# Performance work log

Measured on AMD Instinct MI355X. Metric: run time of the kernel, lower is better.

The kernel has to match this reference:

```python
import jax, jax.numpy as jnp
import numpy as np

B, N, E, D = 2, 8192, 1024, 128   # batch, seq, embed_dim, expand_ratio (= head dim)
H = E // D                        # 8 heads (f_proj output dim)
CHUNK = 64
LN_EPS = 1e-5


def _gla_chunked(q, k, v, log_f):
    """Chunked simple GLA: S_t = exp(log_f_t) * S_{t-1} + k_t v_t^T ; o_t = q_t @ S_t.
    q,k,v: [b,h,n,d], log_f: [b,h,n] (log of per-head scalar decay in (0,1))."""
    b, h, n, d = q.shape
    nc = n // CHUNK
    qc = q.reshape(b, h, nc, CHUNK, d)
    kc = k.reshape(b, h, nc, CHUNK, d)
    vc = v.reshape(b, h, nc, CHUNK, d)
    gf = log_f.reshape(b, h, nc, CHUNK)
    g = jnp.cumsum(gf, axis=-1)          # inclusive within-chunk cum log decay [b,h,nc,C]
    gl = g[..., -1]                      # total chunk log decay [b,h,nc]

    # intra-chunk: A[i,j] = (q_i . k_j) * exp(g_i - g_j), j <= i  (g decreasing -> stable)
    mask = jnp.tril(jnp.ones((CHUNK, CHUNK), bool))
    A = jnp.einsum('bhcid,bhcjd->bhcij', qc, kc)
    A = jnp.where(mask, A * jnp.exp(g[..., :, None] - g[..., None, :]), 0.0)
    o_intra = jnp.einsum('bhcij,bhcjd->bhcid', A, vc)

    # inter-chunk: scan over chunks carrying state S [b,h,d,d]
    def step(S, inp):
        q_c, k_c, v_c, g_c, gl_c = inp   # [b,h,C,d],[b,h,C,d],[b,h,C,d],[b,h,C],[b,h]
        o = jnp.einsum('bhid,bhde->bhie', q_c * jnp.exp(g_c)[..., None], S)
        kd = k_c * jnp.exp(gl_c[..., None] - g_c)[..., None]
        S = jnp.exp(gl_c)[..., None, None] * S + jnp.einsum('bhid,bhie->bhde', kd, v_c)
        return S, o

    xs = (jnp.moveaxis(qc, 2, 0), jnp.moveaxis(kc, 2, 0), jnp.moveaxis(vc, 2, 0),
          jnp.moveaxis(g, 2, 0), jnp.moveaxis(gl, 2, 0))
    S0 = jnp.zeros((b, h, d, d), q.dtype)
    _, o_inter = jax.lax.scan(step, S0, xs)      # [nc,b,h,C,d]
    o_inter = jnp.moveaxis(o_inter, 0, 2)        # [b,h,nc,C,d]
    return (o_intra + o_inter).reshape(b, h, n, d)


def setup_inputs() -> dict:
    key = jax.random.key(0)
    ks = jax.random.split(key, 13)
    s = E ** -0.5
    x = jax.random.normal(ks[0], (B, N, E), jnp.float32)
    # per-head lower bound in (0,1), stored in log space as consumed by the module
    log_lower_bound = jnp.log(jax.random.uniform(ks[1], (H,), jnp.float32, 0.05, 0.95))
    Wq = jax.random.normal(ks[2], (E, E), jnp.float32) * s
    Wk = jax.random.normal(ks[3], (E, E), jnp.float32) * s
    Wv = jax.random.normal(ks[4], (E, E), jnp.float32) * s
    Wf = jax.random.normal(ks[5], (E, H), jnp.float32) * s
    Wb1 = jax.random.normal(ks[6], (E, D), jnp.float32) * s
    Wb2 = jax.random.normal(ks[7], (D, E), jnp.float32) * (D ** -0.5)
    Wg1 = jax.random.normal(ks[8], (E, D), jnp.float32) * s
    Wg2 = jax.random.normal(ks[9], (D, E), jnp.float32) * (D ** -0.5)
    Wo = jax.random.normal(ks[10], (E, E), jnp.float32) * s
    ln_scale = jnp.ones((E,), jnp.float32)
    ln_bias = jnp.zeros((E,), jnp.float32)
    return dict(x=x, log_lower_bound=log_lower_bound, Wq=Wq, Wk=Wk, Wv=Wv, Wf=Wf,
                Wb1=Wb1, Wb2=Wb2, Wg1=Wg1, Wg2=Wg2, Wo=Wo,
                ln_scale=ln_scale, ln_bias=ln_bias)


def reference(x, log_lower_bound, Wq, Wk, Wv, Wf, Wb1, Wb2, Wg1, Wg2, Wo, ln_scale, ln_bias):
    silu = jax.nn.silu
    q = silu(x @ Wq)
    k = silu(x @ Wk)
    v = x @ Wv
    f_pre = x @ Wf                               # [B,N,H] per-head decay logits

    # dense-memory Householder-style reflection of q
    beta = silu((x @ Wb1) @ Wb2)
    nb = jnp.sqrt(jnp.sum(beta * beta, axis=-1, keepdims=True))
    beta = beta / jnp.maximum(nb, 1e-6) / (E ** 0.5)
    q = q - 2.0 * jnp.sum(q * beta, axis=-1, keepdims=True) * beta

    def split(t):
        return t.reshape(B, N, H, D).transpose(0, 2, 1, 3)   # [B,H,N,D]
    qh, kh, vh = split(q), split(k), split(v)

    lb = jnp.exp(log_lower_bound)                            # [H]
    f = lb + (1.0 - lb) * jax.nn.sigmoid(f_pre)              # [B,N,H]
    log_f = jnp.log(f).transpose(0, 2, 1)                    # [B,H,N]

    o = _gla_chunked(qh, kh, vh, log_f)                      # [B,H,N,D]
    o = o.transpose(0, 2, 1, 3).reshape(B, N, E)

    gate = jax.nn.sigmoid((x @ Wg1) @ Wg2)
    o = o * gate

    mu = jnp.mean(o, axis=-1, keepdims=True)
    var = jnp.var(o, axis=-1, keepdims=True)
    o = (o - mu) / jnp.sqrt(var + LN_EPS) * ln_scale + ln_bias
    return o @ Wo
```

## Files before the change

kernel.cpp:

```cpp
#include <hip/hip_runtime.h>
#include <hip/hip_bf16.h>
#include <cstdint>


using u16 = unsigned short;
using u32 = unsigned int;
using u64 = unsigned long long;

typedef __attribute__((ext_vector_type(8))) short s16x8;
typedef __attribute__((ext_vector_type(4))) float f32x4;

__device__ __forceinline__ float b2f(u16 b){ u32 u = ((u32)b)<<16; return __builtin_bit_cast(float,u); }
__device__ __forceinline__ u16 f2b(float f){
  u32 u = __builtin_bit_cast(u32,f);
  return (u16)((u + 0x7FFFu + ((u>>16)&1u)) >> 16);
}
__device__ __forceinline__ float sigm(float x){ return 1.f/(1.f + __expf(-x)); }
__device__ __forceinline__ float silu(float x){ return x * sigm(x); }

__device__ __forceinline__ void gload16(const void* g, void* l){
  __builtin_amdgcn_global_load_lds((const __attribute__((address_space(1))) void*)g,
                                   (__attribute__((address_space(3))) void*)l, 16, 0, 0);
}
#define MFMA(a,b,c) __builtin_amdgcn_mfma_f32_16x16x32_bf16((a),(b),(c),0,0,0)

__device__ __forceinline__ void bar(){
  asm volatile("" ::: "memory");
  __builtin_amdgcn_s_barrier();
  asm volatile("" ::: "memory");
}
__device__ __forceinline__ void wv4(){
  asm volatile("s_waitcnt vmcnt(4)" ::: "memory");
  __builtin_amdgcn_sched_barrier(0);
}
__device__ __forceinline__ void wv0(){
  asm volatile("s_waitcnt vmcnt(0)" ::: "memory");
  __builtin_amdgcn_sched_barrier(0);
}
__device__ __forceinline__ void wv8(){
  asm volatile("s_waitcnt vmcnt(8)" ::: "memory");
  __builtin_amdgcn_sched_barrier(0);
}

__device__ __forceinline__ void swz_block(int& bx, int& by){
  const int gx = gridDim.x;
  const int nwg = gx * gridDim.y;
  int lin = by*gx + bx;
  const int cpx = nwg >> 3;
  lin = (lin & 7)*cpx + (lin >> 3);
  bx = lin % gx; by = lin / gx;
}

__global__ __launch_bounds__(256) void fill_diag(float* __restrict__ p, int n, float val){
  int i = blockIdx.x*256 + threadIdx.x;
  if (i < n) p[i] = val;
}

__global__ __launch_bounds__(256) void cast_bf(const float4* __restrict__ src,
                                               ushort4* __restrict__ dst, int n4){
  int i = blockIdx.x*256 + threadIdx.x;
  int st = gridDim.x*256;
  for (; i < n4; i += st){
    float4 v = src[i];
    ushort4 o; o.x=f2b(v.x); o.y=f2b(v.y); o.z=f2b(v.z); o.w=f2b(v.w);
    dst[i] = o;
  }
}

__global__ __launch_bounds__(256) void wprep_all(const float* __restrict__ Wq,
                                                 const float* __restrict__ Wk,
                                                 const float* __restrict__ Wv,
                                                 const float* __restrict__ Wf,
                                                 const float* __restrict__ Wb1,
                                                 const float* __restrict__ Wb2,
                                                 const float* __restrict__ Wg1,
                                                 const float* __restrict__ Wg2,
                                                 const float* __restrict__ Wo,
                                                 u16* __restrict__ WCAT,
                                                 u16* __restrict__ WB2T,
                                                 u16* __restrict__ WG2T,
                                                 u16* __restrict__ WOT){
  const int z = blockIdx.z;
  const float* src; u16* dst; int K, Nsrc, kb, nb;
  switch(z){
    case 0: src=Wq;  dst=WCAT;            K=1024; Nsrc=1024; kb=16; nb=16; break;
    case 1: src=Wk;  dst=WCAT+1024*1024;  K=1024; Nsrc=1024; kb=16; nb=16; break;
    case 2: src=Wv;  dst=WCAT+2048*1024;  K=1024; Nsrc=1024; kb=16; nb=16; break;
    case 3: src=Wb1; dst=WCAT+3072*1024;  K=1024; Nsrc=128;  kb=16; nb=2;  break;
    case 4: src=Wg1; dst=WCAT+3200*1024;  K=1024; Nsrc=128;  kb=16; nb=2;  break;
    case 5: src=Wf;  dst=WCAT+3328*1024;  K=1024; Nsrc=8;    kb=16; nb=2;  break;
    case 6: src=Wb2; dst=WB2T;            K=128;  Nsrc=1024; kb=2;  nb=16; break;
    case 7: src=Wg2; dst=WG2T;            K=128;  Nsrc=1024; kb=2;  nb=16; break;
    default:src=Wo;  dst=WOT;             K=1024; Nsrc=1024; kb=16; nb=16; break;
  }
  if (blockIdx.x >= (u32)kb || blockIdx.y >= (u32)nb) return;
  __shared__ float t[64][65];
  const int k0 = blockIdx.x*64, n0 = blockIdx.y*64;
  const int tid = threadIdx.x;
  #pragma unroll
  for (int e=0;e<16;e++){
    int idx = e*256 + tid;
    int r = idx>>6, c = idx&63;
    float v = 0.f;
    if (n0 + c < Nsrc) v = src[(u64)(k0+r)*Nsrc + n0 + c];
    t[r][c] = v;
  }
  __syncthreads();
  #pragma unroll
  for (int e=0;e<16;e++){
    int idx = e*256 + tid;
    int nn = idx>>6, kk = idx&63;
    dst[(u64)(n0+nn)*K + k0 + kk] = f2b(t[kk][nn]);
  }
}

__global__ __launch_bounds__(256,4) void gemm_bt(const u16* __restrict__ A, int lda,
                                                 const u16* __restrict__ Bt,
                                                 void* __restrict__ C, int ldc,
                                                 int K, int mode){
  __shared__ __align__(16) u16 As[128*64];
  __shared__ __align__(16) u16 Bs[128*64];
  const int tid = threadIdx.x, lane = tid&63, wid = tid>>6;
  int bx = blockIdx.x, by = blockIdx.y;
  swz_block(bx, by);
  const int bn0 = bx*128, bm0 = by*128;
  const int wr = wid>>1, wc = wid&1;
  const int g = lane>>4, ln = lane&15;

  f32x4 acc[4][4];
  #pragma unroll
  for (int i=0;i<4;i++)
    #pragma unroll
    for (int j=0;j<4;j++) acc[i][j] = f32x4{0.f,0.f,0.f,0.f};

  const int nk = K >> 6;
  for (int kt = 0; kt < nk; ++kt){
    const int k0 = kt<<6;
    #pragma unroll
    for (int j=0;j<4;j++){
      const int p = (wid*4+j)*64 + lane;
      const int row = p>>3, sl = p&7;
      const int sc = ((sl ^ (row&7))<<3);
      gload16(A  + (u64)(bm0+row)*lda + k0 + sc, (char*)As + (wid*4+j)*1024);
      gload16(Bt + (u64)(bn0+row)*K   + k0 + sc, (char*)Bs + (wid*4+j)*1024);
    }
    __syncthreads();
    #pragma unroll
    for (int ks=0;ks<2;ks++){
      s16x8 af[4], bf[4];
      #pragma unroll
      for (int mt=0;mt<4;mt++){
        const int row = wr*64 + mt*16 + ln;
        af[mt] = *(const s16x8*)(As + row*64 + (((ks*4+g) ^ (row&7))<<3));
      }
      #pragma unroll
      for (int nt=0;nt<4;nt++){
        const int row = wc*64 + nt*16 + ln;
        bf[nt] = *(const s16x8*)(Bs + row*64 + (((ks*4+g) ^ (row&7))<<3));
      }
      #pragma unroll
      for (int mt=0;mt<4;mt++)
        #pragma unroll
        for (int nt=0;nt<4;nt++)
          acc[mt][nt] = MFMA(af[mt], bf[nt], acc[mt][nt]);
    }
    __syncthreads();
  }
  if (mode == 0){
    float* Cf = (float*)C;
    #pragma unroll
    for (int mt=0;mt<4;mt++)
      #pragma unroll
      for (int nt=0;nt<4;nt++){
        const int col = bn0 + wc*64 + nt*16 + ln;
        #pragma unroll
        for (int r=0;r<4;r++)
          Cf[(u64)(bm0 + wr*64 + mt*16 + g*4 + r)*ldc + col] = acc[mt][nt][r];
      }
  } else {
    u16* Cb = (u16*)C;
    #pragma unroll
    for (int mt=0;mt<4;mt++)
      #pragma unroll
      for (int nt=0;nt<4;nt++){
        const int col = bn0 + wc*64 + nt*16 + ln;
        #pragma unroll
        for (int r=0;r<4;r++)
          Cb[(u64)(bm0 + wr*64 + mt*16 + g*4 + r)*ldc + col] = f2b(acc[mt][nt][r]);
      }
  }
}

#define STAGE_H(kt_, b_, gb_, ld_, grow0_, loff_)                              \
  do{ const int kk0_ = (kt_)<<6;                                               \
    _Pragma("unroll")                                                          \
    for (int j_=0;j_<2;j_++){                                                  \
      const int p_ = j_*512 + tid;                                             \
      const int row_ = p_>>3, sl_ = p_&7;                                      \
      const int sc_ = ((sl_ ^ (row_&7))<<3);                                   \
      gload16((gb_) + (u64)((grow0_)+row_)*(ld_) + kk0_ + sc_,                 \
              (char*)lds + (b_)*65536 + (loff_) + j_*8192 + wid*1024);         \
    } }while(0)

#define PHASE(mh_, nh_, W_, SG_)                                               \
  do{                                                                          \
    if (W_) wv4();                                                             \
    bar();                                                                     \
    const u16* Ab_ = lds + cbuf*32768 + (mh_)*8192;                            \
    const u16* Bb_ = lds + cbuf*32768 + 16384 + (nh_)*8192;                    \
    s16x8 af_[2][4], bf_[2][2];                                                \
    _Pragma("unroll")                                                          \
    for (int ks=0;ks<2;ks++){                                                  \
      _Pragma("unroll")                                                        \
      for (int m=0;m<4;m++){                                                   \
        const int r_ = wr*64 + m*16 + ln;                                      \
        af_[ks][m] = *(const s16x8*)(Ab_ + r_*64 + (((ks*4+g) ^ (r_&7))<<3));  \
      }                                                                        \
      _Pragma("unroll")                                                        \
      for (int n=0;n<2;n++){                                                   \
        const int r_ = wc*32 + n*16 + ln;                                      \
        bf_[ks][n] = *(const s16x8*)(Bb_ + r_*64 + (((ks*4+g) ^ (r_&7))<<3));  \
      }                                                                        \
    }                                                                          \
    SG_;                                                                       \
    __builtin_amdgcn_s_setprio(1);                                             \
    _Pragma("unroll")                                                          \
    for (int ks=0;ks<2;ks++)                                                   \
      _Pragma("unroll")                                                        \
      for (int m=0;m<4;m++)                                                    \
        _Pragma("unroll")                                                      \
        for (int n=0;n<2;n++)                                                  \
          acc[(mh_)*4+m][(nh_)*2+n] =                                          \
            MFMA(af_[ks][m], bf_[ks][n], acc[(mh_)*4+m][(nh_)*2+n]);           \
    __builtin_amdgcn_s_setprio(0);                                             \
  }while(0)

#define GEMM8P_CORE()                                                          \
  f32x4 acc[8][4];                                                             \
  _Pragma("unroll")                                                            \
  for (int i=0;i<8;i++)                                                        \
    _Pragma("unroll")                                                          \
    for (int j=0;j<4;j++) acc[i][j] = f32x4{0.f,0.f,0.f,0.f};                  \
  const int nk = K >> 6;                                                       \
  STAGE_H(0,0,Bt,K,  bn0,     32768);                                          \
  STAGE_H(0,0,A, lda,bm0,     0);                                              \
  STAGE_H(0,0,Bt,K,  bn0+128, 49152);                                          \
  STAGE_H(0,0,A, lda,bm0+128, 16384);                                          \
  for (int kt=0; kt<nk-1; ++kt){                                               \
    const int cbuf = kt&1, nb = cbuf^1;                                        \
    PHASE(0,0,1, STAGE_H(kt+1,nb,Bt,K,  bn0,     32768));                      \
    PHASE(0,1,1, STAGE_H(kt+1,nb,A, lda,bm0,     0));                          \
    PHASE(1,1,1, STAGE_H(kt+1,nb,Bt,K,  bn0+128, 49152));                      \
    PHASE(1,0,0, STAGE_H(kt+1,nb,A, lda,bm0+128, 16384));                      \
  }                                                                            \
  { const int cbuf = (nk-1)&1;                                                 \
    wv0();                                                                     \
    PHASE(0,0,0,);                                                             \
    PHASE(0,1,0,);                                                             \
    PHASE(1,1,0,);                                                             \
    PHASE(1,0,0,); }

__global__ __launch_bounds__(512,2) void gemm256(const u16* __restrict__ A, int lda,
                                                 const u16* __restrict__ Bt,
                                                 void* __restrict__ C, int ldc,
                                                 int K, int mode){
  __shared__ __align__(16) u16 lds[2*32768];
  const int tid = threadIdx.x, lane = tid&63, wid = tid>>6;
  int bx = blockIdx.x, by = blockIdx.y;
  swz_block(bx, by);
  const int bn0 = bx*256, bm0 = by*256;
  const int wr = (wid>>2), wc = wid&3;
  const int g = lane>>4, ln = lane&15;
  GEMM8P_CORE();
  if (mode == 0){
    float* Cf = (float*)C;
    #pragma unroll
    for (int mh=0;mh<2;mh++)
      #pragma unroll
      for (int m=0;m<4;m++)
        #pragma unroll
        for (int nh=0;nh<2;nh++)
          #pragma unroll
          for (int n=0;n<2;n++){
            const int col = bn0 + nh*128 + wc*32 + n*16 + ln;
            #pragma unroll
            for (int r=0;r<4;r++)
              Cf[(u64)(bm0 + mh*128 + wr*64 + m*16 + g*4 + r)*ldc + col] =
                acc[mh*4+m][nh*2+n][r];
          }
  } else {
    u16* Cb = (u16*)C;
    #pragma unroll
    for (int mh=0;mh<2;mh++)
      #pragma unroll
      for (int m=0;m<4;m++)
        #pragma unroll
        for (int nh=0;nh<2;nh++)
          #pragma unroll
          for (int n=0;n<2;n++){
            const int col = bn0 + nh*128 + wc*32 + n*16 + ln;
            #pragma unroll
            for (int r=0;r<4;r++)
              Cb[(u64)(bm0 + mh*128 + wr*64 + m*16 + g*4 + r)*ldc + col] =
                f2b(acc[mh*4+m][nh*2+n][r]);
          }
  }
}

__global__ __launch_bounds__(512,2) void gemm_proj(const u16* __restrict__ A,
                                                   const u16* __restrict__ Bt,
                                                   u16* __restrict__ Qb,
                                                   u16* __restrict__ Kp,
                                                   u16* __restrict__ KT,
                                                   u16* __restrict__ VT,
                                                   u16* __restrict__ FP,
                                                   const float* __restrict__ Gp,
                                                   const float* __restrict__ GLp){
  __shared__ __align__(16) u16 lds[2*32768];
  const int tid = threadIdx.x, lane = tid&63, wid = tid>>6;
  int bx = blockIdx.x, by = blockIdx.y;
  swz_block(bx, by);
  const int bn0 = bx*256, bm0 = by*256;
  const int lda = 1024, K = 1024;
  const int wr = (wid>>2), wc = wid&3;
  const int g = lane>>4, ln = lane&15;
  GEMM8P_CORE();

  #pragma unroll
  for (int nh=0;nh<2;nh++){
    const int hb2 = (bn0>>7) + nh;
    if (hb2 < 8){
      #pragma unroll
      for (int mh=0;mh<2;mh++)
        #pragma unroll
        for (int m=0;m<4;m++)
          #pragma unroll
          for (int n=0;n<2;n++){
            const int col = bn0 + nh*128 + wc*32 + n*16 + ln;
            #pragma unroll
            for (int r=0;r<4;r++)
              Qb[(u64)(bm0 + mh*128 + wr*64 + m*16 + g*4 + r)*1024 + col] =
                f2b(acc[mh*4+m][nh*2+n][r]);
          }
    } else if (hb2 < 16){
      const int h = hb2 - 8;
      const int bh = (bm0>>13)*8 + h;
      #pragma unroll
      for (int mh=0;mh<2;mh++)
        #pragma unroll
        for (int m=0;m<4;m++){
          const int trowb = (bm0&8191) + mh*128 + wr*64 + m*16 + g*4;
          const float gl = GLp[bh*128 + (trowb>>6)];
          float es[4];
          #pragma unroll
          for (int r=0;r<4;r++) es[r] = __expf(gl - Gp[(u64)bh*8192 + trowb + r]);
          #pragma unroll
          for (int n=0;n<2;n++){
            const int d = wc*32 + n*16 + ln;
            ushort4 o; u16* op = (u16*)&o;
            #pragma unroll
            for (int r=0;r<4;r++){
              const float s = silu(acc[mh*4+m][nh*2+n][r]);
              op[r] = f2b(s * es[r]);
              Kp[(u64)(bm0 + mh*128 + wr*64 + m*16 + g*4 + r)*1024 + h*128 + d] = f2b(s);
            }
            *(ushort4*)(KT + ((u64)bh*128 + d)*8192 + trowb) = o;
          }
        }
    } else if (hb2 < 24){
      const int h = hb2 - 16;
      const int bh = (bm0>>13)*8 + h;
      #pragma unroll
      for (int mh=0;mh<2;mh++)
        #pragma unroll
        for (int m=0;m<4;m++){
          const int trowb = (bm0&8191) + mh*128 + wr*64 + m*16 + g*4;
          #pragma unroll
          for (int n=0;n<2;n++){
            const int d = wc*32 + n*16 + ln;
            ushort4 o; u16* op = (u16*)&o;
            #pragma unroll
            for (int r=0;r<4;r++) op[r] = f2b(acc[mh*4+m][nh*2+n][r]);
            *(ushort4*)(VT + ((u64)bh*128 + d)*8192 + trowb) = o;
          }
        }
    } else {
      #pragma unroll
      for (int mh=0;mh<2;mh++)
        #pragma unroll
        for (int m=0;m<4;m++)
          #pragma unroll
          for (int n=0;n<2;n++){
            const int col = bn0 + nh*128 + wc*32 + n*16 + ln - 3072;
            #pragma unroll
            for (int r=0;r<4;r++)
              FP[(u64)(bm0 + mh*128 + wr*64 + m*16 + g*4 + r)*384 + col] =
                f2b(acc[mh*4+m][nh*2+n][r]);
          }
    }
  }
}

__global__ __launch_bounds__(64) void fkernel(const u16* __restrict__ FP,
                                              const float* __restrict__ llb,
                                              float* __restrict__ G, float* __restrict__ GL){
  const int c = blockIdx.x, bh = blockIdx.y;
  const int b = bh>>3, h = bh&7;
  const int t = threadIdx.x;
  const int tok = c*64 + t;
  const float fp = b2f(FP[(u64)(b*8192 + tok)*384 + 256 + h]);
  const float lb = __expf(llb[h]);
  const float f = lb + (1.f - lb) * sigm(fp);
  float x = __logf(f);
  #pragma unroll
  for (int d=1; d<64; d<<=1){
    float v = __shfl_up(x, d);
    if (t >= d) x += v;
  }
  G[(u64)bh*8192 + tok] = x;
  const float gl = __shfl(x, 63);
  if (t == 0) GL[bh*128 + c] = gl;
}

__global__ __launch_bounds__(256) void e1_reflect(u16* __restrict__ Q,
                                                  const u16* __restrict__ BP){
  const u64 t = blockIdx.x;
  const int tid = threadIdx.x;
  __shared__ float red[8];
  u16* qrow = Q + t*1024;
  const u16* brow = BP + t*1024;
  ushort4 qv = ((const ushort4*)qrow)[tid];
  ushort4 bv = ((const ushort4*)brow)[tid];
  u16* qp = (u16*)&qv; const u16* bp = (const u16*)&bv;
  float q[4], bb[4];
  float s1 = 0.f, s2 = 0.f;
  #pragma unroll
  for (int j=0;j<4;j++){
    const float qq = silu(b2f(qp[j]));
    const float bbv = silu(b2f(bp[j]));
    q[j] = qq; bb[j] = bbv;
    s1 += bbv*bbv; s2 += qq*bbv;
  }
  #pragma unroll
  for (int d=1; d<64; d<<=1){ s1 += __shfl_xor(s1,d); s2 += __shfl_xor(s2,d); }
  const int wid = tid>>6, lane = tid&63;
  if (lane==0){ red[wid]=s1; red[4+wid]=s2; }
  __syncthreads();
  s1 = red[0]+red[1]+red[2]+red[3];
  s2 = red[4]+red[5]+red[6]+red[7];
  const float bs = 1.f/(fmaxf(sqrtf(s1), 1e-6f) * 32.f);
  const float coef = 2.f * s2 * bs * bs;
  #pragma unroll
  for (int j=0;j<4;j++) qp[j] = f2b(q[j] - coef*bb[j]);
  ((ushort4*)qrow)[tid] = qv;
}

__global__ __launch_bounds__(256,4) void g1_local(const u16* __restrict__ KT,
                                                  const u16* __restrict__ VT,
                                                  u16* __restrict__ LT){
  __shared__ __align__(16) u16 kts[128*64];
  __shared__ __align__(16) u16 vts[128*64];
  const int c = blockIdx.x, bh = blockIdx.y;
  const int tid = threadIdx.x, lane = tid&63, wid = tid>>6;
  const int g = lane>>4, ln = lane&15;
  #pragma unroll
  for (int j=0;j<4;j++){
    const int p = (wid*4+j)*64 + lane;
    const int row = p>>3, sl = p&7;
    const int sc = ((sl ^ (row&7))<<3);
    gload16(KT + ((u64)bh*128 + row)*8192 + (u64)c*64 + sc, (char*)kts + (wid*4+j)*1024);
    gload16(VT + ((u64)bh*128 + row)*8192 + (u64)c*64 + sc, (char*)vts + (wid*4+j)*1024);
  }
  __syncthreads();
  f32x4 acc[2][8];
  #pragma unroll
  for (int mt=0;mt<2;mt++)
    #pragma unroll
    for (int dt=0;dt<8;dt++) acc[mt][dt] = f32x4{0.f,0.f,0.f,0.f};
  #pragma unroll
  for (int kk=0;kk<2;kk++){
    s16x8 av[2];
    #pragma unroll
    for (int mt=0;mt<2;mt++){
      const int row = wid*32 + mt*16 + ln;
      av[mt] = *(const s16x8*)(vts + row*64 + (((kk*4+g) ^ (row&7))<<3));
    }
    #pragma unroll
    for (int dt=0;dt<8;dt++){
      const int row = dt*16 + ln;
      const s16x8 bk = *(const s16x8*)(kts + row*64 + (((kk*4+g) ^ (row&7))<<3));
      #pragma unroll
      for (int mt=0;mt<2;mt++) acc[mt][dt] = MFMA(av[mt], bk, acc[mt][dt]);
    }
  }
  u16* out = LT + ((u64)(bh*128 + c)<<14);
  #pragma unroll
  for (int mt=0;mt<2;mt++)
    #pragma unroll
    for (int dt=0;dt<8;dt++){
      const int d = dt*16 + ln;
      #pragma unroll
      for (int r=0;r<4;r++){
        const int n = wid*32 + mt*16 + g*4 + r;
        out[n*128 + d] = f2b(acc[mt][dt][r]);
      }
    }
}

__global__ __launch_bounds__(256) void g2_scan(u16* __restrict__ LS,
                                               const float* __restrict__ GL){
  __shared__ float egl[128];
  const int bh = blockIdx.y;
  if (threadIdx.x < 128) egl[threadIdx.x] = __expf(GL[bh*128 + threadIdx.x]);
  __syncthreads();
  const u64 e = (u64)blockIdx.x*256 + threadIdx.x;
  u16* P = LS + ((u64)bh<<21) + e;
  float s = 0.f;
  for (int c=0;c<128;c++){
    const float l = b2f(P[(u64)c<<14]);
    P[(u64)c<<14] = f2b(s);
    s = egl[c]*s + l;
  }
}

__global__ __launch_bounds__(256,2) void g3_out(const u16* __restrict__ Qb,
                                                const u16* __restrict__ Kp,
                                                const u16* __restrict__ VT,
                                                const u16* __restrict__ SBb,
                                                const float* __restrict__ Gb,
                                                u16* __restrict__ O){
  __shared__ __align__(16) u16 qs[64*128];
  __shared__ __align__(16) u16 ks[64*128];
  __shared__ __align__(16) u16 vts[128*64];
  __shared__ __align__(16) u16 sbs[64*128];
  __shared__ __align__(16) u16 Ast[4][16*64];
  __shared__ float gg[64];
  const int c = blockIdx.x, bh = blockIdx.y;
  const int b = bh>>3, h = bh&7;
  const int tid = threadIdx.x, lane = tid&63, wid = tid>>6;
  const int g = lane>>4, ln = lane&15;
  const u64 trow0 = (u64)b*8192 + (u64)c*64;

  if (tid < 64) gg[tid] = Gb[(u64)bh*8192 + c*64 + tid];

  const u16* sbbase = SBb + ((u64)(bh*128 + c)<<14);
  #pragma unroll
  for (int j=0;j<4;j++){
    const int p = (wid*4+j)*64 + lane;
    const int row = p>>4, sl = p&15;
    const int sc = ((sl ^ (row&7))<<3);
    gload16(Qb + (trow0 + row)*1024 + h*128 + sc, (char*)qs + (wid*4+j)*1024);
    gload16(Kp + (trow0 + row)*1024 + h*128 + sc, (char*)ks + (wid*4+j)*1024);
    const int row2 = p>>3, sl2 = p&7;
    gload16(VT + ((u64)bh*128 + row2)*8192 + (u64)c*64 + ((sl2 ^ (row2&7))<<3),
            (char*)vts + (wid*4+j)*1024);
    gload16(sbbase + row*128 + sc, (char*)sbs + (wid*4+j)*1024);
  }
  __syncthreads();

  f32x4 pa[4];
  #pragma unroll
  for (int jt=0;jt<4;jt++) pa[jt] = f32x4{0.f,0.f,0.f,0.f};
  #pragma unroll
  for (int kk=0;kk<4;kk++){
    const int arow = wid*16 + ln;
    const s16x8 aq = *(const s16x8*)(qs + arow*128 + (((kk*4+g) ^ (arow&7))<<3));
    #pragma unroll
    for (int jt=0;jt<4;jt++){
      const int brow = jt*16 + ln;
      const s16x8 bk = *(const s16x8*)(ks + brow*128 + (((kk*4+g) ^ (brow&7))<<3));
      pa[jt] = MFMA(aq, bk, pa[jt]);
    }
  }
  #pragma unroll
  for (int jt=0;jt<4;jt++){
    const int jj = jt*16 + ln;
    const float gj = gg[jj];
    #pragma unroll
    for (int r=0;r<4;r++){
      const int il = g*4 + r;
      const int ii = wid*16 + il;
      const float v = (jj <= ii) ? pa[jt][r] * __expf(gg[ii] - gj) : 0.f;
      Ast[wid][il*64 + (((jj>>3) ^ (il&7))<<3) + (jj&7)] = f2b(v);
    }
  }
  {
    const int row = wid*16 + (lane>>2);
    const float sc = __expf(gg[row]);
    u16* base = qs + row*128 + (lane&3)*32;
    #pragma unroll
    for (int ee=0; ee<4; ee++){
      s16x8 v = *(s16x8*)(base + ee*8);
      u16* vp = (u16*)&v;
      #pragma unroll
      for (int xj=0;xj<8;xj++) vp[xj] = f2b(b2f(vp[xj]) * sc);
      *(s16x8*)(base + ee*8) = v;
    }
  }
  f32x4 acc[8];
  #pragma unroll
  for (int i=0;i<8;i++) acc[i] = f32x4{0.f,0.f,0.f,0.f};
  #pragma unroll
  for (int kk=0;kk<2;kk++){
    const s16x8 aa = *(const s16x8*)(Ast[wid] + ln*64 + (((kk*4+g) ^ (ln&7))<<3));
    #pragma unroll
    for (int nt=0;nt<8;nt++){
      const int brow = nt*16 + ln;
      const s16x8 bb = *(const s16x8*)(vts + brow*64 + (((kk*4+g) ^ (brow&7))<<3));
      acc[nt] = MFMA(aa, bb, acc[nt]);
    }
  }
  #pragma unroll
  for (int kk=0;kk<4;kk++){
    const int arow = wid*16 + ln;
    const s16x8 aq = *(const s16x8*)(qs + arow*128 + (((kk*4+g) ^ (arow&7))<<3));
    #pragma unroll
    for (int nt=0;nt<4;nt++){
      const int brow = nt*16 + ln;
      const s16x8 bs = *(const s16x8*)(sbs + brow*128 + (((kk*4+g) ^ (brow&7))<<3));
      acc[nt] = MFMA(aq, bs, acc[nt]);
    }
  }
  __syncthreads();
  #pragma unroll
  for (int j=0;j<4;j++){
    const int p = (wid*4+j)*64 + lane;
    const int row = p>>4, sl = p&15;
    gload16(sbbase + 8192 + row*128 + ((sl ^ (row&7))<<3), (char*)sbs + (wid*4+j)*1024);
  }
  __syncthreads();
  #pragma unroll
  for (int kk=0;kk<4;kk++){
    const int arow = wid*16 + ln;
    const s16x8 aq = *(const s16x8*)(qs + arow*128 + (((kk*4+g) ^ (arow&7))<<3));
    #pragma unroll
    for (int nt=0;nt<4;nt++){
      const int brow = nt*16 + ln;
      const s16x8 bs = *(const s16x8*)(sbs + brow*128 + (((kk*4+g) ^ (brow&7))<<3));
      acc[4+nt] = MFMA(aq, bs, acc[4+nt]);
    }
  }
  u16* outp = O + trow0*1024 + h*128;
  #pragma unroll
  for (int nt=0;nt<8;nt++){
    const int n = nt*16 + ln;
    #pragma unroll
    for (int r=0;r<4;r++){
      const int i = wid*16 + g*4 + r;
      outp[(u64)i*1024 + n] = f2b(acc[nt][r]);
    }
  }
}

__global__ __launch_bounds__(256) void e2_ln(const u16* __restrict__ O,
                                             const u16* __restrict__ GP,
                                             const float* __restrict__ lnsc,
                                             const float* __restrict__ lnbi,
                                             u16* __restrict__ OL){
  const u64 t = blockIdx.x;
  const int tid = threadIdx.x;
  __shared__ float red[8];
  ushort4 ov = ((const ushort4*)(O + t*1024))[tid];
  ushort4 gv = ((const ushort4*)(GP + t*1024))[tid];
  const u16* ovp = (const u16*)&ov;
  const u16* gvp = (const u16*)&gv;
  float o[4]; float s = 0.f, s2 = 0.f;
  #pragma unroll
  for (int j=0;j<4;j++){
    const float val = b2f(ovp[j]) * sigm(b2f(gvp[j]));
    o[j] = val; s += val; s2 += val*val;
  }
  #pragma unroll
  for (int d=1; d<64; d<<=1){ s += __shfl_xor(s,d); s2 += __shfl_xor(s2,d); }
  const int wid = tid>>6, lane = tid&63;
  if (lane==0){ red[wid]=s; red[4+wid]=s2; }
  __syncthreads();
  s = red[0]+red[1]+red[2]+red[3];
  s2 = red[4]+red[5]+red[6]+red[7];
  const float mu = s * (1.f/1024.f);
  const float var = s2 * (1.f/1024.f) - mu*mu;
  const float rs = rsqrtf(var + 1e-5f);
  ushort4 out; u16* op = (u16*)&out;
  #pragma unroll
  for (int j=0;j<4;j++){
    const int e = tid*4 + j;
    op[j] = f2b((o[j]-mu)*rs*lnsc[e] + lnbi[e]);
  }
  ((ushort4*)(OL + t*1024))[tid] = out;
}

extern "C" void kernel_launch(void* const* d_in, const int* in_sizes, int n_in,
                              void* d_out, int out_size, void* d_ws, size_t ws_size,
                              hipStream_t stream){
  const float* x   = (const float*)d_in[0];
  const float* llb = (const float*)d_in[1];
  const float* Wq  = (const float*)d_in[2];
  const float* Wk  = (const float*)d_in[3];
  const float* Wv  = (const float*)d_in[4];
  const float* Wf  = (const float*)d_in[5];
  const float* Wb1 = (const float*)d_in[6];
  const float* Wb2 = (const float*)d_in[7];
  const float* Wg1 = (const float*)d_in[8];
  const float* Wg2 = (const float*)d_in[9];
  const float* Wo  = (const float*)d_in[10];
  const float* lnsc= (const float*)d_in[11];
  const float* lnbi= (const float*)d_in[12];

  const u64 REQUIRED = 190586880ull;
  if (ws_size < REQUIRED){
    const float val = 1.0e6f + (float)(u64)(ws_size>>20) * 1024.0f;
    fill_diag<<<dim3((out_size+255)/256),256,0,stream>>>((float*)d_out, out_size, val);
    return;
  }

  char* ws = (char*)d_ws;
  u16*  WCAT = (u16*)(ws + 0ull);
  u16*  WB2T = (u16*)(ws + 7077888ull);
  u16*  WG2T = (u16*)(ws + 7340032ull);
  u16*  WOT  = (u16*)(ws + 7602176ull);
  float* Gb  = (float*)(ws + 9699328ull);
  float* GLb = (float*)(ws + 10223616ull);
  u16*  FP   = (u16*)(ws + 10231808ull);
  u16*  R0   = (u16*)(ws + 22814720ull);
  u16*  Qb   = (u16*)(ws + 56369152ull);
  u16*  Kp   = (u16*)(ws + 89923584ull);
  u16*  KT   = (u16*)(ws + 123478016ull);
  u16*  VT   = (u16*)(ws + 157032448ull);
  u16*  LTSB = (u16*)d_out;
  u16*  XB = R0, *BP = R0, *GP = R0;
  u16*  Ob = KT, *OL = Qb;

  cast_bf<<<dim3(4096),256,0,stream>>>((const float4*)x, (ushort4*)XB, 16384*1024/4);
  wprep_all<<<dim3(16,16,9),256,0,stream>>>(Wq,Wk,Wv,Wf,Wb1,Wb2,Wg1,Wg2,Wo,
                                            WCAT, WB2T, WG2T, WOT);

  gemm_bt<<<dim3(1,128),256,0,stream>>>(XB, 1024, WCAT + 3328*1024, FP + 256, 384, 1024, 1);
  fkernel<<<dim3(128,16),64,0,stream>>>(FP, llb, Gb, GLb);

  gemm_proj<<<dim3(13,64),512,0,stream>>>(XB, WCAT, Qb, Kp, KT, VT, FP, Gb, GLb);

  gemm256<<<dim3(4,64),512,0,stream>>>(FP, 384, WB2T, BP, 1024, 128, 1);
  e1_reflect<<<dim3(16384),256,0,stream>>>(Qb, BP);

  gemm256<<<dim3(4,64),512,0,stream>>>(FP + 128, 384, WG2T, GP, 1024, 128, 1);

  g1_local<<<dim3(128,16),256,0,stream>>>(KT, VT, LTSB);
  g2_scan<<<dim3(64,16),256,0,stream>>>(LTSB, GLb);
  g3_out<<<dim3(128,16),256,0,stream>>>(Qb, Kp, VT, LTSB, Gb, Ob);

  e2_ln<<<dim3(16384),256,0,stream>>>(Ob, GP, lnsc, lnbi, OL);

  gemm256<<<dim3(4,64),512,0,stream>>>(OL, 1024, WOT, d_out, 1024, 1024, 0);
}
```

Baseline: 380.1 us.

## Restructure 256x256 GEMM main loop: per-warp contiguous quadrants, wait-all pipeline

Reworks the shared GEMM core used by gemm256 and the fused projection kernel. Each warp now owns a contiguous 128x64 output region instead of interleaved halves. The loop issues LDS reads, then the next-tile global-to-LDS stage, then a barrier, lgkmcnt(0) wait and the MFMAs. The old staggered vmcnt(4) waits give way to one vmcnt(0) wait plus barrier per K step. This aims to simplify synchronisation and improve LDS read locality, but the full vmcnt(0) wait per iteration may expose more global-load latency than the old staggered waits.

```diff
diff --git a/kernel.cpp b/kernel.cpp
--- a/kernel.cpp
+++ b/kernel.cpp
@@ -29,16 +29,12 @@
   __builtin_amdgcn_s_barrier();
   asm volatile("" ::: "memory");
 }
-__device__ __forceinline__ void wv4(){
-  asm volatile("s_waitcnt vmcnt(4)" ::: "memory");
-  __builtin_amdgcn_sched_barrier(0);
-}
 __device__ __forceinline__ void wv0(){
   asm volatile("s_waitcnt vmcnt(0)" ::: "memory");
   __builtin_amdgcn_sched_barrier(0);
 }
-__device__ __forceinline__ void wv8(){
-  asm volatile("s_waitcnt vmcnt(8)" ::: "memory");
+__device__ __forceinline__ void lgkm0(){
+  asm volatile("s_waitcnt lgkmcnt(0)" ::: "memory");
   __builtin_amdgcn_sched_barrier(0);
 }
 
@@ -202,27 +198,26 @@
               (char*)lds + (b_)*65536 + (loff_) + j_*8192 + wid*1024);         \
     } }while(0)
 
-#define PHASE(mh_, nh_, W_, SG_)                                               \
-  do{                                                                          \
-    if (W_) wv4();                                                             \
-    bar();                                                                     \
-    const u16* Ab_ = lds + cbuf*32768 + (mh_)*8192;                            \
-    const u16* Bb_ = lds + cbuf*32768 + 16384 + (nh_)*8192;                    \
+#define DSREAD_PH(qm_, qn_)                                                    \
     s16x8 af_[2][4], bf_[2][2];                                                \
-    _Pragma("unroll")                                                          \
-    for (int ks=0;ks<2;ks++){                                                  \
+    { const u16* Ab_ = lds + cbuf*32768 + wr*8192;                             \
+      const u16* Bb_ = lds + cbuf*32768 + 16384 + (wc>>1)*8192;                \
       _Pragma("unroll")                                                        \
-      for (int m=0;m<4;m++){                                                   \
-        const int r_ = wr*64 + m*16 + ln;                                      \
-        af_[ks][m] = *(const s16x8*)(Ab_ + r_*64 + (((ks*4+g) ^ (r_&7))<<3));  \
-      }                                                                        \
-      _Pragma("unroll")                                                        \
-      for (int n=0;n<2;n++){                                                   \
-        const int r_ = wc*32 + n*16 + ln;                                      \
-        bf_[ks][n] = *(const s16x8*)(Bb_ + r_*64 + (((ks*4+g) ^ (r_&7))<<3));  \
-      }                                                                        \
-    }                                                                          \
-    SG_;                                                                       \
+      for (int ks=0;ks<2;ks++){                                                \
+        _Pragma("unroll")                                                      \
+        for (int m=0;m<4;m++){                                                 \
+          const int r_ = (qm_)*64 + m*16 + ln;                                 \
+          af_[ks][m] = *(const s16x8*)(Ab_ + r_*64 + (((ks*4+g) ^ (ln&7))<<3));\
+        }                                                                      \
+        _Pragma("unroll")                                                      \
+        for (int n=0;n<2;n++){                                                 \
+          const int r_ = (wc&1)*64 + (qn_)*32 + n*16 + ln;                     \
+          bf_[ks][n] = *(const s16x8*)(Bb_ + r_*64 + (((ks*4+g) ^ (ln&7))<<3));\
+        }                                                                      \
+      } }
+
+#define MFMA_PH(qm_, qn_)                                                      \
+    bar(); lgkm0();                                                            \
     __builtin_amdgcn_s_setprio(1);                                             \
     _Pragma("unroll")                                                          \
     for (int ks=0;ks<2;ks++)                                                   \
@@ -230,12 +225,11 @@
       for (int m=0;m<4;m++)                                                    \
         _Pragma("unroll")                                                      \
         for (int n=0;n<2;n++)                                                  \
-          acc[(mh_)*4+m][(nh_)*2+n] =                                          \
-            MFMA(af_[ks][m], bf_[ks][n], acc[(mh_)*4+m][(nh_)*2+n]);           \
-    __builtin_amdgcn_s_setprio(0);                                             \
-  }while(0)
-
-#define GEMM8P_CORE()                                                          \
+          acc[(qm_)*4+m][(qn_)*2+n] =                                          \
+            MFMA(af_[ks][m], bf_[ks][n], acc[(qm_)*4+m][(qn_)*2+n]);           \
+    __builtin_amdgcn_s_setprio(0);
+
+#define GEMMP_CORE()                                                           \
   f32x4 acc[8][4];                                                             \
   _Pragma("unroll")                                                            \
   for (int i=0;i<8;i++)                                                        \
@@ -246,19 +240,21 @@
   STAGE_H(0,0,A, lda,bm0,     0);                                              \
   STAGE_H(0,0,Bt,K,  bn0+128, 49152);                                          \
   STAGE_H(0,0,A, lda,bm0+128, 16384);                                          \
-  for (int kt=0; kt<nk-1; ++kt){                                               \
-    const int cbuf = kt&1, nb = cbuf^1;                                        \
-    PHASE(0,0,1, STAGE_H(kt+1,nb,Bt,K,  bn0,     32768));                      \
-    PHASE(0,1,1, STAGE_H(kt+1,nb,A, lda,bm0,     0));                          \
-    PHASE(1,1,1, STAGE_H(kt+1,nb,Bt,K,  bn0+128, 49152));                      \
-    PHASE(1,0,0, STAGE_H(kt+1,nb,A, lda,bm0+128, 16384));                      \
-  }                                                                            \
-  { const int cbuf = (nk-1)&1;                                                 \
-    wv0();                                                                     \
-    PHASE(0,0,0,);                                                             \
-    PHASE(0,1,0,);                                                             \
-    PHASE(1,1,0,);                                                             \
-    PHASE(1,0,0,); }
+  wv0(); bar();                                                                \
+  for (int kt=0; kt<nk; ++kt){                                                 \
+    const int cbuf = kt&1, nbuf = cbuf^1;                                      \
+    const bool st = (kt+1 < nk);                                               \
+    { DSREAD_PH(0,0); if(st) STAGE_H(kt+1,nbuf,Bt,K,  bn0,     32768);         \
+      MFMA_PH(0,0); }                                                          \
+    { DSREAD_PH(0,1); if(st) STAGE_H(kt+1,nbuf,A, lda,bm0,     0);             \
+      MFMA_PH(0,1); }                                                          \
+    { DSREAD_PH(1,0); if(st) STAGE_H(kt+1,nbuf,Bt,K,  bn0+128, 49152);         \
+      MFMA_PH(1,0); }                                                          \
+    { DSREAD_PH(1,1); if(st) STAGE_H(kt+1,nbuf,A, lda,bm0+128, 16384);         \
+      MFMA_PH(1,1); }                                                          \
+    if (st) wv0();                                                             \
+    bar();                                                                     \
+  }
 
 __global__ __launch_bounds__(512,2) void gemm256(const u16* __restrict__ A, int lda,
                                                  const u16* __restrict__ Bt,
@@ -269,40 +265,40 @@
   int bx = blockIdx.x, by = blockIdx.y;
   swz_block(bx, by);
   const int bn0 = bx*256, bm0 = by*256;
-  const int wr = (wid>>2), wc = wid&3;
+  const int wr = wid>>2, wc = wid&3;
   const int g = lane>>4, ln = lane&15;
-  GEMM8P_CORE();
+  GEMMP_CORE();
   if (mode == 0){
     float* Cf = (float*)C;
     #pragma unroll
-    for (int mh=0;mh<2;mh++)
+    for (int qm=0;qm<2;qm++)
       #pragma unroll
       for (int m=0;m<4;m++)
         #pragma unroll
-        for (int nh=0;nh<2;nh++)
+        for (int qn=0;qn<2;qn++)
           #pragma unroll
           for (int n=0;n<2;n++){
-            const int col = bn0 + nh*128 + wc*32 + n*16 + ln;
+            const int col = bn0 + wc*64 + qn*32 + n*16 + ln;
             #pragma unroll
             for (int r=0;r<4;r++)
-              Cf[(u64)(bm0 + mh*128 + wr*64 + m*16 + g*4 + r)*ldc + col] =
-                acc[mh*4+m][nh*2+n][r];
+              Cf[(u64)(bm0 + wr*128 + qm*64 + m*16 + g*4 + r)*ldc + col] =
+                acc[qm*4+m][qn*2+n][r];
           }
   } else {
     u16* Cb = (u16*)C;
     #pragma unroll
-    for (int mh=0;mh<2;mh++)
+    for (int qm=0;qm<2;qm++)
       #pragma unroll
       for (int m=0;m<4;m++)
         #pragma unroll
-        for (int nh=0;nh<2;nh++)
+        for (int qn=0;qn<2;qn++)
           #pragma unroll
           for (int n=0;n<2;n++){
-            const int col = bn0 + nh*128 + wc*32 + n*16 + ln;
+            const int col = bn0 + wc*64 + qn*32 + n*16 + ln;
             #pragma unroll
             for (int r=0;r<4;r++)
-              Cb[(u64)(bm0 + mh*128 + wr*64 + m*16 + g*4 + r)*ldc + col] =
-                f2b(acc[mh*4+m][nh*2+n][r]);
+              Cb[(u64)(bm0 + wr*128 + qm*64 + m*16 + g*4 + r)*ldc + col] =
+                f2b(acc[qm*4+m][qn*2+n][r]);
           }
   }
 }
@@ -322,82 +318,88 @@
   swz_block(bx, by);
   const int bn0 = bx*256, bm0 = by*256;
   const int lda = 1024, K = 1024;
-  const int wr = (wid>>2), wc = wid&3;
+  const int wr = wid>>2, wc = wid&3;
   const int g = lane>>4, ln = lane&15;
-  GEMM8P_CORE();
-
-  #pragma unroll
-  for (int nh=0;nh<2;nh++){
-    const int hb2 = (bn0>>7) + nh;
-    if (hb2 < 8){
-      #pragma unroll
-      for (int mh=0;mh<2;mh++)
-        #pragma unroll
-        for (int m=0;m<4;m++)
+  GEMMP_CORE();
+
+  const int hb2 = (bn0>>7) + (wc>>1);
+  const int dq  = (wc&1)*64;
+  if (hb2 < 8){
+    #pragma unroll
+    for (int qm=0;qm<2;qm++)
+      #pragma unroll
+      for (int m=0;m<4;m++)
+        #pragma unroll
+        for (int qn=0;qn<2;qn++)
           #pragma unroll
           for (int n=0;n<2;n++){
-            const int col = bn0 + nh*128 + wc*32 + n*16 + ln;
+            const int col = bn0 + wc*64 + qn*32 + n*16 + ln;
             #pragma unroll
             for (int r=0;r<4;r++)
-              Qb[(u64)(bm0 + mh*128 + wr*64 + m*16 + g*4 + r)*1024 + col] =
-                f2b(acc[mh*4+m][nh*2+n][r]);
+              Qb[(u64)(bm0 + wr*128 + qm*64 + m*16 + g*4 + r)*1024 + col] =
+                f2b(acc[qm*4+m][qn*2+n][r]);
           }
-    } else if (hb2 < 16){
-      const int h = hb2 - 8;
-      const int bh = (bm0>>13)*8 + h;
-      #pragma unroll
-      for (int mh=0;mh<2;mh++)
-        #pragma unroll
-        for (int m=0;m<4;m++){
-          const int trowb = (bm0&8191) + mh*128 + wr*64 + m*16 + g*4;
-          const float gl = GLp[bh*128 + (trowb>>6)];
-          float es[4];
-          #pragma unroll
-          for (int r=0;r<4;r++) es[r] = __expf(gl - Gp[(u64)bh*8192 + trowb + r]);
+  } else if (hb2 < 16){
+    const int h = hb2 - 8;
+    const int bh = (bm0>>13)*8 + h;
+    #pragma unroll
+    for (int qm=0;qm<2;qm++)
+      #pragma unroll
+      for (int m=0;m<4;m++){
+        const int trow = (bm0&8191) + wr*128 + qm*64 + m*16 + g*4;
+        const float gl = GLp[bh*128 + (trow>>6)];
+        float es[4];
+        #pragma unroll
+        for (int r=0;r<4;r++) es[r] = __expf(gl - Gp[(u64)bh*8192 + trow + r]);
+        #pragma unroll
+        for (int qn=0;qn<2;qn++)
           #pragma unroll
           for (int n=0;n<2;n++){
-            const int d = wc*32 + n*16 + ln;
+            const int d = dq + qn*32 + n*16 + ln;
             ushort4 o; u16* op = (u16*)&o;
             #pragma unroll
             for (int r=0;r<4;r++){
-              const float s = silu(acc[mh*4+m][nh*2+n][r]);
+              const float s = silu(acc[qm*4+m][qn*2+n][r]);
               op[r] = f2b(s * es[r]);
-              Kp[(u64)(bm0 + mh*128 + wr*64 + m*16 + g*4 + r)*1024 + h*128 + d] = f2b(s);
+              Kp[(u64)(bm0 + wr*128 + qm*64 + m*16 + g*4 + r)*1024 + h*128 + d] = f2b(s);
             }
-            *(ushort4*)(KT + ((u64)bh*128 + d)*8192 + trowb) = o;
+            *(ushort4*)(KT + ((u64)bh*128 + d)*8192 + trow) = o;
           }
-        }
-    } else if (hb2 < 24){
-      const int h = hb2 - 16;
-      const int bh = (bm0>>13)*8 + h;
-      #pragma unroll
-      for (int mh=0;mh<2;mh++)
-        #pragma unroll
-        for (int m=0;m<4;m++){
-          const int trowb = (bm0&8191) + mh*128 + wr*64 + m*16 + g*4;
+      }
+  } else if (hb2 < 24){
+    const int h = hb2 - 16;
+    const int bh = (bm0>>13)*8 + h;
+    #pragma unroll
+    for (int qm=0;qm<2;qm++)
+      #pragma unroll
+      for (int m=0;m<4;m++){
+        const int trow = (bm0&8191) + wr*128 + qm*64 + m*16 + g*4;
+        #pragma unroll
+        for (int qn=0;qn<2;qn++)
           #pragma unroll
           for (int n=0;n<2;n++){
-            const int d = wc*32 + n*16 + ln;
+            const int d = dq + qn*32 + n*16 + ln;
             ushort4 o; u16* op = (u16*)&o;
             #pragma unroll
-            for (int r=0;r<4;r++) op[r] = f2b(acc[mh*4+m][nh*2+n][r]);
-            *(ushort4*)(VT + ((u64)bh*128 + d)*8192 + trowb) = o;
+            for (int r=0;r<4;r++) op[r] = f2b(acc[qm*4+m][qn*2+n][r]);
+            *(ushort4*)(VT + ((u64)bh*128 + d)*8192 + trow) = o;
           }
-        }
-    } else {
-      #pragma unroll
-      for (int mh=0;mh<2;mh++)
-        #pragma unroll
-        for (int m=0;m<4;m++)
+      }
+  } else {
+    #pragma unroll
+    for (int qm=0;qm<2;qm++)
+      #pragma unroll
+      for (int m=0;m<4;m++)
+        #pragma unroll
+        for (int qn=0;qn<2;qn++)
           #pragma unroll
           for (int n=0;n<2;n++){
-            const int col = bn0 + nh*128 + wc*32 + n*16 + ln - 3072;
+            const int col = bn0 + wc*64 + qn*32 + n*16 + ln - 3072;
             #pragma unroll
             for (int r=0;r<4;r++)
-              FP[(u64)(bm0 + mh*128 + wr*64 + m*16 + g*4 + r)*384 + col] =
-                f2b(acc[mh*4+m][nh*2+n][r]);
+              FP[(u64)(bm0 + wr*128 + qm*64 + m*16 + g*4 + r)*384 + col] =
+                f2b(acc[qm*4+m][qn*2+n][r]);
           }
-    }
   }
 }
 
```

New measurement: 384.0 us. Within noise of the previous version (+1.0%).
